# Kernel tuning notes

Measured on AMD Instinct MI355X. Metric: run time of the kernel, lower is better.

The kernel has to match this reference:

```python
import jax, jax.numpy as jnp
import numpy as np

IN_DIM = 256
OUT_DIM = 64
NUM_HEADS = 4
N = 6144


def setup_inputs() -> dict:
    key = jax.random.key(0)
    ks = jax.random.split(key, 9)
    h = jax.random.normal(ks[0], (N, IN_DIM), dtype=jnp.float32)
    # dense multiplicative adjacency weights, one [N,N] matrix per head
    adj = jax.random.uniform(ks[1], (NUM_HEADS, N, N), dtype=jnp.float32)
    s = 1.0 / np.sqrt(IN_DIM)
    WQ = jax.random.normal(ks[2], (NUM_HEADS, IN_DIM, OUT_DIM), dtype=jnp.float32) * s
    WK = jax.random.normal(ks[3], (NUM_HEADS, IN_DIM, OUT_DIM), dtype=jnp.float32) * s
    WV = jax.random.normal(ks[4], (NUM_HEADS, IN_DIM, OUT_DIM), dtype=jnp.float32) * s
    bQ = jax.random.normal(ks[5], (NUM_HEADS, OUT_DIM), dtype=jnp.float32) * 0.01
    bK = jax.random.normal(ks[6], (NUM_HEADS, OUT_DIM), dtype=jnp.float32) * 0.01
    bV = jax.random.normal(ks[7], (NUM_HEADS, OUT_DIM), dtype=jnp.float32) * 0.01
    return {"adj": adj, "h": h, "WQ": WQ, "bQ": bQ, "WK": WK, "bK": bK, "WV": WV, "bV": bV}


def reference(adj, h, WQ, bQ, WK, bK, WV, bV):
    # Per-head projections, batched over heads: [H, N, out_dim]
    Qh = jnp.einsum('nd,hdo->hno', h, WQ) + bQ[:, None, :]
    Kh = jnp.einsum('nd,hdo->hno', h, WK) + bK[:, None, :]
    Vh = jnp.einsum('nd,hdo->hno', h, WV) + bV[:, None, :]
    scale = 1.0 / jnp.sqrt(jnp.asarray(h.shape[1], dtype=h.dtype))
    # multiplicative adjacency mask (NOT additive) applied before softmax
    A_tilde = scale * jnp.einsum('hno,hmo->hnm', Qh, Kh) * adj  # [H, N, N]
    attention = jax.nn.softmax(A_tilde, axis=-1)
    X = jnp.einsum('hnm,hmo->hno', attention, Vh)  # [H, N, out_dim]
    return X
```

## Files before the change

kernel.cpp:

```cpp
#include <hip/hip_runtime.h>
#include <hip/hip_bf16.h>

#define NN 6144
#define HEADS 4
#define DIN 256
#define DOUT 64

typedef __bf16 bf16_t;
typedef bf16_t bf16x8 __attribute__((ext_vector_type(8)));
typedef float f32x16 __attribute__((ext_vector_type(16)));
typedef float f32x4 __attribute__((ext_vector_type(4)));
typedef unsigned u32x4 __attribute__((ext_vector_type(4)));

#if __has_builtin(__builtin_amdgcn_exp2f)
#define EXP2(x) __builtin_amdgcn_exp2f(x)
#else
#define EXP2(x) exp2f(x)
#endif

static __device__ __forceinline__ f32x16 zero16() {
  f32x16 z;
#pragma unroll
  for (int i = 0; i < 16; ++i) z[i] = 0.0f;
  return z;
}

static __device__ __forceinline__ bf16x8 ldg8(const bf16_t* p) {
  return *reinterpret_cast<const bf16x8*>(p);
}

static __device__ __forceinline__ unsigned pk2(float a, float b) {
  union { bf16_t h[2]; unsigned u; } z;
  z.h[0] = (bf16_t)a;
  z.h[1] = (bf16_t)b;
  return z.u;
}

static __device__ __forceinline__ void pswap(unsigned& x, unsigned& y) {
  asm("v_permlane32_swap_b32 %0, %1" : "+v"(x), "+v"(y));
}

static __device__ __forceinline__ f32x4 ldnt4(const float* p) {
  return __builtin_nontemporal_load(reinterpret_cast<const f32x4*>(p));
}

#define SCHED0() __builtin_amdgcn_sched_barrier(0)

__global__ __launch_bounds__(256) void prep_kernel(
    const float* __restrict__ h, const float* __restrict__ WQ,
    const float* __restrict__ WK, const float* __restrict__ WV,
    bf16_t* __restrict__ hb, bf16_t* __restrict__ Wt) {
  int stride = gridDim.x * blockDim.x;
  int idx = blockIdx.x * blockDim.x + threadIdx.x;
  for (int i = idx; i < NN * DIN; i += stride)
    hb[i] = (bf16_t)h[i];
  const float c2 = 0.0625f * 1.4426950408889634f;
  for (int i = idx; i < 3 * HEADS * DOUT * DIN; i += stride) {
    int d = i & (DIN - 1);
    int o = (i >> 8) & (DOUT - 1);
    int hh = (i >> 14) & (HEADS - 1);
    int m = i >> 16;
    const float* W = (m == 0) ? WQ : (m == 1) ? WK : WV;
    float v = W[(hh * DIN + d) * DOUT + o];
    if (m == 0) v *= c2;
    Wt[i] = (bf16_t)v;
  }
}

__global__ __launch_bounds__(256) void proj_kernel(
    const bf16_t* __restrict__ hb, const bf16_t* __restrict__ Wt,
    const float* __restrict__ bQ, const float* __restrict__ bK,
    const float* __restrict__ bV,
    bf16_t* __restrict__ Qb, bf16_t* __restrict__ Kf, bf16_t* __restrict__ Vf) {
  const float c2 = 0.0625f * 1.4426950408889634f;
  int tid = threadIdx.x;
  int w = tid >> 6, l = tid & 63;
  int l31 = l & 31, lh = l >> 5;
  int hh = blockIdx.y;
  int n0 = blockIdx.x * 64;

#pragma unroll
  for (int s = 0; s < 3; ++s) {
    int t = w * 3 + s;
    if (t < 8) {
      int m = t >> 2;
      int rh = (t >> 1) & 1;
      int oh = t & 1;
      const bf16_t* arow = hb + (n0 + rh * 32 + l31) * DIN + 8 * lh;
      const bf16_t* brow = Wt + ((m * HEADS + hh) * DOUT + oh * 32 + l31) * DIN + 8 * lh;
      f32x16 acc = zero16();
#pragma unroll
      for (int kc = 0; kc < 16; ++kc)
        acc = __builtin_amdgcn_mfma_f32_32x32x16_bf16(ldg8(arow + kc * 16),
                                                      ldg8(brow + kc * 16), acc, 0, 0, 0);
      const float* bias = (m == 0) ? bQ : bK;
      float bv = bias[hh * DOUT + oh * 32 + l31];
      if (m == 0) {
        bv *= c2;
        bf16_t* outp = Qb + (size_t)(hh * NN + n0 + rh * 32) * DOUT + oh * 32 + l31;
#pragma unroll
        for (int r = 0; r < 16; ++r) {
          int q = (r & 3) + 8 * (r >> 2) + 4 * lh;
          outp[q * DOUT] = (bf16_t)(acc[r] + bv);
        }
      } else {
        int o = oh * 32 + l31;
        bf16_t* outp = Kf + (size_t)hh * 393216 + (n0 >> 6) * 4096 + rh * 2048 +
                       (o >> 4) * 512 + ((o >> 3) & 1) * 256 + (o & 7);
#pragma unroll
        for (int r = 0; r < 16; ++r) {
          int rr = (r & 3) + 8 * (r >> 2) + 4 * lh;
          outp[rr * 8] = (bf16_t)(acc[r] + bv);
        }
      }
    } else {
      int tt = t - 8;
      int oh = tt >> 1, nh = tt & 1;
      const bf16_t* arow = Wt + ((2 * HEADS + hh) * DOUT + oh * 32 + l31) * DIN + 8 * lh;
      const bf16_t* brow = hb + (n0 + nh * 32 + l31) * DIN + 8 * lh;
      f32x16 acc = zero16();
#pragma unroll
      for (int kc = 0; kc < 16; ++kc)
        acc = __builtin_amdgcn_mfma_f32_32x32x16_bf16(ldg8(arow + kc * 16),
                                                      ldg8(brow + kc * 16), acc, 0, 0, 0);
      int k6 = nh * 32 + l31;
      bf16_t* outp = Vf + (size_t)hh * 393216 + (n0 >> 6) * 4096 + oh * 2048 +
                     (k6 >> 4) * 512 + ((k6 >> 3) & 1) * 256 + (k6 & 7);
#pragma unroll
      for (int r = 0; r < 16; ++r) {
        int rr = (r & 3) + 8 * (r >> 2) + 4 * lh;
        float bvv = bV[hh * DOUT + oh * 32 + rr];
        outp[rr * 8] = (bf16_t)(acc[r] + bvv);
      }
    }
  }
}

__global__ __launch_bounds__(256, 2) void attn_kernel(
    const float* __restrict__ adj, const bf16_t* __restrict__ Qb,
    const bf16_t* __restrict__ Kf, const bf16_t* __restrict__ Vf,
    float* __restrict__ out) {
  __shared__ __align__(16) float smem[2][32][256];

  int tid = threadIdx.x;
  int w = tid >> 6, l = tid & 63;
  int l31 = l & 31, lh = l >> 5;

  int bid = blockIdx.x;
  int work = (bid & 7) * 96 + (bid >> 3);
  int hh = work / 192;
  int q0 = (work % 192) * 32;

  const bf16_t* Qrow = Qb + (size_t)(hh * NN + q0 + l31) * DOUT + 8 * lh;
  bf16x8 qf[4];
#pragma unroll
  for (int kc = 0; kc < 4; ++kc) qf[kc] = ldg8(Qrow + kc * 16);

  const bf16_t* Kh = Kf + (size_t)hh * 393216;
  const bf16_t* Vh = Vf + (size_t)hh * 393216;
  const float* adjq = adj + (size_t)hh * NN * NN + (size_t)q0 * NN;

  f32x16 o0 = zero16(), o1 = zero16();
  float sacc = 0.0f;

  f32x4 areg[8];

#pragma unroll
  for (int i = 0; i < 8; ++i) {
    int row = 8 * w + i;
    areg[i] = ldnt4(adjq + (size_t)row * NN + ((l ^ i) << 2));
  }
  asm volatile("s_waitcnt vmcnt(0)" ::: "memory");
  SCHED0();
#pragma unroll
  for (int i = 0; i < 8; ++i) {
    int row = 8 * w + i;
    *reinterpret_cast<f32x4*>(&smem[0][row][l << 2]) = areg[i];
  }
  asm volatile("s_waitcnt lgkmcnt(0)" ::: "memory");
  SCHED0();
  __builtin_amdgcn_s_barrier();
  SCHED0();

  for (int it = 0; it < 24; ++it) {
    int cur = it & 1;
    int chunk = it * 4 + w;

    const bf16_t* kbase = Kh + (size_t)chunk * 4096 + l * 8;
    const bf16_t* vbase = Vh + (size_t)chunk * 4096 + l * 8;
    bf16x8 kf[8], vf[8];
#pragma unroll
    for (int x = 0; x < 4; ++x) {
      kf[x] = ldg8(kbase + x * 512);
      kf[4 + x] = ldg8(kbase + 2048 + x * 512);
    }
#pragma unroll
    for (int x = 0; x < 4; ++x) {
      vf[x] = ldg8(vbase + x * 512);
      vf[4 + x] = ldg8(vbase + 2048 + x * 512);
    }
    SCHED0();

    int nt = (it + 1 < 24) ? it + 1 : 23;
#pragma unroll
    for (int i = 0; i < 8; ++i) {
      int row = 8 * w + i;
      areg[i] = ldnt4(adjq + (size_t)row * NN + nt * 256 + ((l ^ i) << 2));
    }
    SCHED0();

    f32x4 av[8];
#pragma unroll
    for (int t2 = 0; t2 < 2; ++t2)
#pragma unroll
      for (int g = 0; g < 4; ++g) {
        int c = 16 * w + 8 * t2 + 2 * g + lh;
        av[t2 * 4 + g] =
            *reinterpret_cast<const f32x4*>(&smem[cur][l31][(c ^ (l31 & 7)) << 2]);
      }

    f32x16 s0 = zero16(), s1 = zero16();
#pragma unroll
    for (int kc = 0; kc < 4; ++kc) {
      s0 = __builtin_amdgcn_mfma_f32_32x32x16_bf16(kf[kc], qf[kc], s0, 0, 0, 0);
      s1 = __builtin_amdgcn_mfma_f32_32x32x16_bf16(kf[4 + kc], qf[kc], s1, 0, 0, 0);
    }

#pragma unroll
    for (int t2 = 0; t2 < 2; ++t2) {
      f32x16 st = t2 ? s1 : s0;
      float p[16];
#pragma unroll
      for (int r = 0; r < 16; ++r) {
        float pv = EXP2(st[r] * av[4 * t2 + (r >> 2)][r & 3]);
        p[r] = pv;
        sacc += pv;
      }
#pragma unroll
      for (int c = 0; c < 2; ++c) {
        unsigned wA0 = pk2(p[8 * c + 0], p[8 * c + 1]);
        unsigned wB0 = pk2(p[8 * c + 2], p[8 * c + 3]);
        unsigned wA1 = pk2(p[8 * c + 4], p[8 * c + 5]);
        unsigned wB1 = pk2(p[8 * c + 6], p[8 * c + 7]);
        pswap(wA0, wA1);
        pswap(wB0, wB1);
        u32x4 pw;
        pw[0] = wA0; pw[1] = wB0; pw[2] = wA1; pw[3] = wB1;
        bf16x8 pb = __builtin_bit_cast(bf16x8, pw);
        int kc = 2 * t2 + c;
        o0 = __builtin_amdgcn_mfma_f32_32x32x16_bf16(vf[kc], pb, o0, 0, 0, 0);
        o1 = __builtin_amdgcn_mfma_f32_32x32x16_bf16(vf[4 + kc], pb, o1, 0, 0, 0);
      }
    }

    asm volatile("s_waitcnt vmcnt(0)" ::: "memory");
    SCHED0();
#pragma unroll
    for (int i = 0; i < 8; ++i) {
      int row = 8 * w + i;
      *reinterpret_cast<f32x4*>(&smem[cur ^ 1][row][l << 2]) = areg[i];
    }
    asm volatile("s_waitcnt lgkmcnt(0)" ::: "memory");
    SCHED0();
    __builtin_amdgcn_s_barrier();
    SCHED0();
  }

  __syncthreads();

  float stot = sacc + __shfl_xor(sacc, 32);
  float* opart = &smem[0][0][0];
  float* ssum = &smem[0][0][0] + 8192;
  if (l < 32) ssum[w * 32 + l31] = stot;
#pragma unroll
  for (int r = 0; r < 16; ++r) {
    int d = (r & 3) + 8 * (r >> 2) + 4 * lh;
    opart[w * 2048 + d * 32 + l31] = o0[r];
    opart[w * 2048 + (32 + d) * 32 + l31] = o1[r];
  }
  __syncthreads();

#pragma unroll
  for (int k = 0; k < 8; ++k) {
    int idx = k * 256 + tid;
    int q = idx & 31, d = idx >> 5;
    float s = ssum[q] + ssum[32 + q] + ssum[64 + q] + ssum[96 + q];
    float ov = opart[d * 32 + q] + opart[2048 + d * 32 + q] +
               opart[4096 + d * 32 + q] + opart[6144 + d * 32 + q];
    out[(size_t)(hh * NN + q0 + q) * DOUT + d] = ov / s;
  }
}

extern "C" void kernel_launch(void* const* d_in, const int* in_sizes, int n_in,
                              void* d_out, int out_size, void* d_ws, size_t ws_size,
                              hipStream_t stream) {
  const float* adj = (const float*)d_in[0];
  const float* h   = (const float*)d_in[1];
  const float* WQ  = (const float*)d_in[2];
  const float* bQ  = (const float*)d_in[3];
  const float* WK  = (const float*)d_in[4];
  const float* bK  = (const float*)d_in[5];
  const float* WV  = (const float*)d_in[6];
  const float* bV  = (const float*)d_in[7];
  float* out = (float*)d_out;

  if (ws_size < 12976128) return;

  char* ws = (char*)d_ws;
  bf16_t* hb = (bf16_t*)ws;
  bf16_t* Wt = (bf16_t*)(ws + 3145728);
  bf16_t* Qb = (bf16_t*)(ws + 3538944);
  bf16_t* Kf = (bf16_t*)(ws + 6684672);
  bf16_t* Vf = (bf16_t*)(ws + 9830400);

  prep_kernel<<<1024, 256, 0, stream>>>(h, WQ, WK, WV, hb, Wt);
  proj_kernel<<<dim3(96, 4), 256, 0, stream>>>(hb, Wt, bQ, bK, bV, Qb, Kf, Vf);
  attn_kernel<<<768, 256, 0, stream>>>(adj, Qb, Kf, Vf, out);
}
```

Baseline: 176.0 us.

## Prefetch adjacency two tiles ahead and stagger each block's starting tile

The attention loop now keeps two register buffers of adjacency data and issues global loads two iterations ahead instead of one. It waits with a partial vmcnt, so the newest prefetch stays in flight while the previous tile is stored to shared memory. Each block also starts its 24-tile sweep at a rotated offset (bid % 24) to spread concurrent DRAM traffic across the adjacency rows. The loop is unrolled by two so the buffers can alternate. The cost is about 32 more live VGPRs per thread, which could limit occupancy or cause spills under the 2-blocks-per-CU launch bound.

```diff
diff --git a/kernel.cpp b/kernel.cpp
--- a/kernel.cpp
+++ b/kernel.cpp
@@ -45,6 +45,9 @@
 }
 
 #define SCHED0() __builtin_amdgcn_sched_barrier(0)
+#define VW(N)                                                   \
+  asm volatile("s_waitcnt vmcnt(" #N ")" ::: "memory");         \
+  SCHED0();
 
 __global__ __launch_bounds__(256) void prep_kernel(
     const float* __restrict__ h, const float* __restrict__ WQ,
@@ -136,6 +139,80 @@
   }
 }
 
+#define ATTN_BODY(AIN, AOUT, IT, CUR)                                          \
+  {                                                                            \
+    int tc = t0 + (IT);                                                        \
+    if (tc >= 24) tc -= 24;                                                    \
+    int tni = t0 + (IT) + 2;                                                   \
+    if (tni >= 24) tni -= 24;                                                  \
+    int chunk = tc * 4 + w;                                                    \
+    const bf16_t* kbase = Kh + (size_t)chunk * 4096 + l * 8;                   \
+    const bf16_t* vbase = Vh + (size_t)chunk * 4096 + l * 8;                   \
+    bf16x8 kf[8], vf[8];                                                       \
+    _Pragma("unroll") for (int x = 0; x < 4; ++x) {                            \
+      kf[x] = ldg8(kbase + x * 512);                                           \
+      kf[4 + x] = ldg8(kbase + 2048 + x * 512);                                \
+    }                                                                          \
+    _Pragma("unroll") for (int x = 0; x < 4; ++x) {                            \
+      vf[x] = ldg8(vbase + x * 512);                                           \
+      vf[4 + x] = ldg8(vbase + 2048 + x * 512);                                \
+    }                                                                          \
+    SCHED0();                                                                  \
+    if ((IT) < 22) {      \
+      _Pragma("unroll") for (int i = 0; i < 8; ++i) {                          \
+        int row = 8 * w + i;                                                   \
+        AOUT[i] = ldnt4(adjq + (size_t)row * NN + tni * 256 + ((l ^ i) << 2)); \
+      }                                                                        \
+    }                                                                          \
+    SCHED0();                                                                  \
+    f32x4 av[8];                                                               \
+    _Pragma("unroll") for (int t2 = 0; t2 < 2; ++t2)                           \
+        _Pragma("unroll") for (int g = 0; g < 4; ++g) {                        \
+      int c = 16 * w + 8 * t2 + 2 * g + lh;                                    \
+      av[t2 * 4 + g] = *reinterpret_cast<const f32x4*>(                        \
+          &smem[CUR][l31][(c ^ (l31 & 7)) << 2]);                              \
+    }                                                                          \
+    f32x16 s0 = zero16(), s1 = zero16();                                       \
+    _Pragma("unroll") for (int kc = 0; kc < 4; ++kc) {                         \
+      s0 = __builtin_amdgcn_mfma_f32_32x32x16_bf16(kf[kc], qf[kc], s0, 0, 0, 0);\
+      s1 = __builtin_amdgcn_mfma_f32_32x32x16_bf16(kf[4 + kc], qf[kc], s1, 0, 0, 0);\
+    }                                                                          \
+    _Pragma("unroll") for (int t2 = 0; t2 < 2; ++t2) {                         \
+      f32x16 st = t2 ? s1 : s0;                                                \
+      float p[16];                                                             \
+      _Pragma("unroll") for (int r = 0; r < 16; ++r) {                         \
+        float pv = EXP2(st[r] * av[4 * t2 + (r >> 2)][r & 3]);                 \
+        p[r] = pv;                                                             \
+        sacc += pv;                                                            \
+      }                                                                        \
+      _Pragma("unroll") for (int c2 = 0; c2 < 2; ++c2) {                       \
+        unsigned wA0 = pk2(p[8 * c2 + 0], p[8 * c2 + 1]);                      \
+        unsigned wB0 = pk2(p[8 * c2 + 2], p[8 * c2 + 3]);                      \
+        unsigned wA1 = pk2(p[8 * c2 + 4], p[8 * c2 + 5]);                      \
+        unsigned wB1 = pk2(p[8 * c2 + 6], p[8 * c2 + 7]);                      \
+        pswap(wA0, wA1);                                                       \
+        pswap(wB0, wB1);                                                       \
+        u32x4 pw;                                                              \
+        pw[0] = wA0; pw[1] = wB0; pw[2] = wA1; pw[3] = wB1;                    \
+        bf16x8 pb = __builtin_bit_cast(bf16x8, pw);                            \
+        int kc = 2 * t2 + c2;                                                  \
+        o0 = __builtin_amdgcn_mfma_f32_32x32x16_bf16(vf[kc], pb, o0, 0, 0, 0); \
+        o1 = __builtin_amdgcn_mfma_f32_32x32x16_bf16(vf[4 + kc], pb, o1, 0, 0, 0);\
+      }                                                                        \
+    }                                                                          \
+    if ((IT) < 23) {          \
+      VW(8)                                                                    \
+      _Pragma("unroll") for (int i = 0; i < 8; ++i) {                          \
+        int row = 8 * w + i;                                                   \
+        *reinterpret_cast<f32x4*>(&smem[(CUR) ^ 1][row][l << 2]) = AIN[i];     \
+      }                                                                        \
+      asm volatile("s_waitcnt lgkmcnt(0)" ::: "memory");                       \
+      SCHED0();                                                                \
+      __builtin_amdgcn_s_barrier();                                           \
+      SCHED0();                                                                \
+    }                                                                          \
+  }
+
 __global__ __launch_bounds__(256, 2) void attn_kernel(
     const float* __restrict__ adj, const bf16_t* __restrict__ Qb,
     const bf16_t* __restrict__ Kf, const bf16_t* __restrict__ Vf,
@@ -150,6 +227,7 @@
   int work = (bid & 7) * 96 + (bid >> 3);
   int hh = work / 192;
   int q0 = (work % 192) * 32;
+  int t0 = bid % 24;
 
   const bf16_t* Qrow = Qb + (size_t)(hh * NN + q0 + l31) * DOUT + 8 * lh;
   bf16x8 qf[4];
@@ -163,109 +241,37 @@
   f32x16 o0 = zero16(), o1 = zero16();
   float sacc = 0.0f;
 
-  f32x4 areg[8];
+  f32x4 aregA[8], aregB[8];
 
 #pragma unroll
   for (int i = 0; i < 8; ++i) {
     int row = 8 * w + i;
-    areg[i] = ldnt4(adjq + (size_t)row * NN + ((l ^ i) << 2));
-  }
-  asm volatile("s_waitcnt vmcnt(0)" ::: "memory");
-  SCHED0();
+    aregA[i] = ldnt4(adjq + (size_t)row * NN + t0 * 256 + ((l ^ i) << 2));
+  }
+  int t1 = t0 + 1;
+  if (t1 >= 24) t1 -= 24;
 #pragma unroll
   for (int i = 0; i < 8; ++i) {
     int row = 8 * w + i;
-    *reinterpret_cast<f32x4*>(&smem[0][row][l << 2]) = areg[i];
+    aregB[i] = ldnt4(adjq + (size_t)row * NN + t1 * 256 + ((l ^ i) << 2));
+  }
+  VW(8)
+#pragma unroll
+  for (int i = 0; i < 8; ++i) {
+    int row = 8 * w + i;
+    *reinterpret_cast<f32x4*>(&smem[0][row][l << 2]) = aregA[i];
   }
   asm volatile("s_waitcnt lgkmcnt(0)" ::: "memory");
   SCHED0();
   __builtin_amdgcn_s_barrier();
   SCHED0();
 
-  for (int it = 0; it < 24; ++it) {
-    int cur = it & 1;
-    int chunk = it * 4 + w;
-
-    const bf16_t* kbase = Kh + (size_t)chunk * 4096 + l * 8;
-    const bf16_t* vbase = Vh + (size_t)chunk * 4096 + l * 8;
-    bf16x8 kf[8], vf[8];
-#pragma unroll
-    for (int x = 0; x < 4; ++x) {
-      kf[x] = ldg8(kbase + x * 512);
-      kf[4 + x] = ldg8(kbase + 2048 + x * 512);
-    }
-#pragma unroll
-    for (int x = 0; x < 4; ++x) {
-      vf[x] = ldg8(vbase + x * 512);
-      vf[4 + x] = ldg8(vbase + 2048 + x * 512);
-    }
-    SCHED0();
-
-    int nt = (it + 1 < 24) ? it + 1 : 23;
-#pragma unroll
-    for (int i = 0; i < 8; ++i) {
-      int row = 8 * w + i;
-      areg[i] = ldnt4(adjq + (size_t)row * NN + nt * 256 + ((l ^ i) << 2));
-    }
-    SCHED0();
-
-    f32x4 av[8];
-#pragma unroll
-    for (int t2 = 0; t2 < 2; ++t2)
-#pragma unroll
-      for (int g = 0; g < 4; ++g) {
-        int c = 16 * w + 8 * t2 + 2 * g + lh;
-        av[t2 * 4 + g] =
-            *reinterpret_cast<const f32x4*>(&smem[cur][l31][(c ^ (l31 & 7)) << 2]);
-      }
-
-    f32x16 s0 = zero16(), s1 = zero16();
-#pragma unroll
-    for (int kc = 0; kc < 4; ++kc) {
-      s0 = __builtin_amdgcn_mfma_f32_32x32x16_bf16(kf[kc], qf[kc], s0, 0, 0, 0);
-      s1 = __builtin_amdgcn_mfma_f32_32x32x16_bf16(kf[4 + kc], qf[kc], s1, 0, 0, 0);
-    }
-
-#pragma unroll
-    for (int t2 = 0; t2 < 2; ++t2) {
-      f32x16 st = t2 ? s1 : s0;
-      float p[16];
-#pragma unroll
-      for (int r = 0; r < 16; ++r) {
-        float pv = EXP2(st[r] * av[4 * t2 + (r >> 2)][r & 3]);
-        p[r] = pv;
-        sacc += pv;
-      }
-#pragma unroll
-      for (int c = 0; c < 2; ++c) {
-        unsigned wA0 = pk2(p[8 * c + 0], p[8 * c + 1]);
-        unsigned wB0 = pk2(p[8 * c + 2], p[8 * c + 3]);
-        unsigned wA1 = pk2(p[8 * c + 4], p[8 * c + 5]);
-        unsigned wB1 = pk2(p[8 * c + 6], p[8 * c + 7]);
-        pswap(wA0, wA1);
-        pswap(wB0, wB1);
-        u32x4 pw;
-        pw[0] = wA0; pw[1] = wB0; pw[2] = wA1; pw[3] = wB1;
-        bf16x8 pb = __builtin_bit_cast(bf16x8, pw);
-        int kc = 2 * t2 + c;
-        o0 = __builtin_amdgcn_mfma_f32_32x32x16_bf16(vf[kc], pb, o0, 0, 0, 0);
-        o1 = __builtin_amdgcn_mfma_f32_32x32x16_bf16(vf[4 + kc], pb, o1, 0, 0, 0);
-      }
-    }
-
-    asm volatile("s_waitcnt vmcnt(0)" ::: "memory");
-    SCHED0();
-#pragma unroll
-    for (int i = 0; i < 8; ++i) {
-      int row = 8 * w + i;
-      *reinterpret_cast<f32x4*>(&smem[cur ^ 1][row][l << 2]) = areg[i];
-    }
-    asm volatile("s_waitcnt lgkmcnt(0)" ::: "memory");
-    SCHED0();
-    __builtin_amdgcn_s_barrier();
-    SCHED0();
-  }
-
+  for (int it2 = 0; it2 < 12; ++it2) {
+    ATTN_BODY(aregB, aregA, 2 * it2, 0)
+    ATTN_BODY(aregA, aregB, 2 * it2 + 1, 1)
+  }
+
+  VW(0)
   __syncthreads();
 
   float stot = sacc + __shfl_xor(sacc, 32);
```

After: 160.9 us. -8.6%, faster.
